# Kernel tuning notes

Measured on AMD Instinct MI355X. Metric: run time of the kernel, lower is better.

## Reference

```python
import jax, jax.numpy as jnp
import numpy as np

L, H, NH, KVH, HD, DFF = 8, 1024, 16, 2, 64, 4096
G = NH // KVH          # kv groups = 8
S, PAST = 256, 2048
T = S + PAST
QKH = NH + KVH         # heads that receive RoPE


def setup_inputs() -> dict:
    key = jax.random.key(0)
    ks = jax.random.split(key, 10)
    w = 0.02
    # causal additive mask: past fully visible, causal within new chunk
    pos = jnp.arange(T)[None, :]
    mask = jnp.where(pos <= PAST + jnp.arange(S)[:, None], 0.0, -1e9).astype(jnp.float32)
    return {
        "hidden_states": jax.random.normal(ks[0], (S, H), jnp.float32),
        "rope_cos": jax.random.uniform(ks[1], (S, 1, HD), jnp.float32, -1.0, 1.0),
        "rope_sin": jax.random.uniform(ks[2], (S, 1, HD), jnp.float32, -1.0, 1.0),
        "attention_mask": mask,
        "past_keys": jax.random.normal(ks[3], (L, KVH, HD, PAST), jnp.float32),
        "past_values": jax.random.normal(ks[4], (L, KVH, PAST, HD), jnp.float32),
        "qkv_w": jax.random.normal(ks[5], (L, (NH + 2 * KVH) * HD, H), jnp.float32) * w,
        "o_w": jax.random.normal(ks[6], (L, H, H), jnp.float32) * w,
        "gate_up_w": jax.random.normal(ks[7], (L, 2 * DFF, H), jnp.float32) * w,
        "down_w": jax.random.normal(ks[8], (L, H, DFF), jnp.float32) * w,
        "norm_w": jnp.ones((H,), jnp.float32),
    }


def _rms_sum(x):
    # faithful to module: rsqrt of SUM of squares (sqrt(H) absorbed into fused weights)
    return x * jax.lax.rsqrt(jnp.sum(x * x, axis=-1, keepdims=True))


def _rotate_half(x):
    # flip-based rotate: swaps halves, NO negation (sign folded into sin input)
    return jnp.concatenate([x[..., HD // 2:], x[..., : HD // 2]], axis=-1)


def reference(hidden_states, rope_cos, rope_sin, attention_mask,
              past_keys, past_values, qkv_w, o_w, gate_up_w, down_w, norm_w):
    def layer(h, p):
        qw, ow, guw, dw, pk, pv = p
        # --- attention ---
        x = _rms_sum(h)
        qkv = (x @ qw.T).reshape(S, NH + 2 * KVH, HD)
        qk, v = qkv[:, :QKH], qkv[:, QKH:]               # [S,QKH,HD], [S,KVH,HD]
        qk = qk * rope_cos + _rotate_half(qk) * rope_sin
        q, k = qk[:, :NH], qk[:, NH:]
        q = q.reshape(S, KVH, G, HD).transpose(1, 2, 0, 3)       # [KVH,G,S,HD]
        K = jnp.concatenate([pk, k.transpose(1, 2, 0)], axis=-1)  # [KVH,HD,T]
        V = jnp.concatenate([pv, v.transpose(1, 0, 2)], axis=-2)  # [KVH,T,HD]
        scores = jnp.einsum('kgsd,kdt->kgst', q, K) + attention_mask
        p_attn = jax.nn.softmax(scores, axis=-1)
        o = jnp.einsum('kgst,ktd->kgsd', p_attn, V)
        o = o.transpose(2, 0, 1, 3).reshape(S, H)
        h = h + o @ ow.T
        # --- fused gate-up MLP (SiLU) ---
        x = _rms_sum(h)
        gu = x @ guw.T
        gate, up = gu[:, :DFF], gu[:, DFF:]
        h = h + (jax.nn.silu(gate) * up) @ dw.T
        return h, (K, V)

    h, _kv = jax.lax.scan(layer, hidden_states,
                          (qkv_w, o_w, gate_up_w, down_w, past_keys, past_values))
    # final RMSNorm (standard, mean-based, with learned weight)
    out = h * jax.lax.rsqrt(jnp.mean(h * h, axis=-1, keepdims=True) + 1e-6) * norm_w
    return out
```

## Files before the change

### kernel.cpp

```cpp
#include <hip/hip_runtime.h>
#include <hip/hip_bf16.h>

typedef __attribute__((ext_vector_type(4))) float f32x4;
typedef __attribute__((ext_vector_type(8))) __bf16 bf16x8;
typedef unsigned short u16;
typedef __attribute__((ext_vector_type(4))) unsigned short u16x4;

__device__ __forceinline__ u16 f2bf(float f) {
  __bf16 h = (__bf16)f;
  return __builtin_bit_cast(u16, h);
}

__device__ __forceinline__ bf16x8 cvt2(f32x4 x, f32x4 y) {
  bf16x8 r;
  r[0] = (__bf16)x[0]; r[1] = (__bf16)x[1]; r[2] = (__bf16)x[2]; r[3] = (__bf16)x[3];
  r[4] = (__bf16)y[0]; r[5] = (__bf16)y[1]; r[6] = (__bf16)y[2]; r[7] = (__bf16)y[3];
  return r;
}

template<int CMODE, int NBK, int MI>
__global__ __launch_bounds__(512) void gemmW(
    const u16* __restrict__ A, const float* __restrict__ B,
    void* __restrict__ Cv, int K, int ldc)
{
  __shared__ char Bl[2][8192];
  int n0 = blockIdx.x * 32;
  int kb = blockIdx.y * (NBK * 128);
  int m0 = blockIdx.z * (MI * 128);
  int tid = threadIdx.x, lane = tid & 63, w = tid >> 6;
  int r0 = lane & 15, g = lane >> 4;
  int trow = tid >> 4, tcol = tid & 15;

  const float* bsrc = B + (long long)(n0 + trow) * K + kb + tcol * 8;
  const u16* abase = A + (long long)(m0 + w * (MI * 16) + r0) * K + kb + g * 8;
  int swr = (trow & 7) << 4;
  int wofs = trow * 256 + ((tcol * 16) ^ swr);

  {
    f32x4 u = *(const f32x4*)bsrc;
    f32x4 v = *(const f32x4*)(bsrc + 4);
    *(bf16x8*)&Bl[0][wofs] = cvt2(u, v);
  }
  bf16x8 a[2][MI][4];
#pragma unroll
  for (int mi = 0; mi < MI; mi++)
#pragma unroll
    for (int kk = 0; kk < 4; kk++)
      a[0][mi][kk] = *(const bf16x8*)(abase + (long long)mi * 16 * K + kk * 32);

  f32x4 acc[MI][2];
#pragma unroll
  for (int i = 0; i < MI; i++)
#pragma unroll
    for (int j = 0; j < 2; j++) acc[i][j] = (f32x4){0.f, 0.f, 0.f, 0.f};

  __syncthreads();

#pragma unroll
  for (int ibk = 0; ibk < NBK; ibk++) {
    const int cur = ibk & 1;
    const int nxt = cur ^ 1;
    f32x4 u, v;
    if (ibk + 1 < NBK) {
      int ko = (ibk + 1) * 128;
#pragma unroll
      for (int mi = 0; mi < MI; mi++)
#pragma unroll
        for (int kk = 0; kk < 4; kk++)
          a[nxt][mi][kk] = *(const bf16x8*)(abase + (long long)mi * 16 * K + ko + kk * 32);
      u = *(const f32x4*)(bsrc + ko);
      v = *(const f32x4*)(bsrc + ko + 4);
    }
    bf16x8 bfr[2][4];
#pragma unroll
    for (int nj = 0; nj < 2; nj++) {
      int row = nj * 16 + r0;
      int rb = row * 256, sw = (row & 7) << 4;
#pragma unroll
      for (int kk = 0; kk < 4; kk++)
        bfr[nj][kk] = *(const bf16x8*)&Bl[cur][rb + ((kk * 64 + g * 16) ^ sw)];
    }
#pragma unroll
    for (int kk = 0; kk < 4; kk++)
#pragma unroll
      for (int mi = 0; mi < MI; mi++)
#pragma unroll
        for (int nj = 0; nj < 2; nj++)
          acc[mi][nj] = __builtin_amdgcn_mfma_f32_16x16x32_bf16(a[cur][mi][kk], bfr[nj][kk], acc[mi][nj], 0, 0, 0);
    if (ibk + 1 < NBK)
      *(bf16x8*)&Bl[nxt][wofs] = cvt2(u, v);
    __syncthreads();
  }

  long long co = (long long)blockIdx.y * 256 * ldc;
  int rr = (lane >> 4) << 2;
#pragma unroll
  for (int mi = 0; mi < MI; mi++)
#pragma unroll
    for (int nj = 0; nj < 2; nj++)
#pragma unroll
      for (int q = 0; q < 4; q++) {
        int row = m0 + w * (MI * 16) + mi * 16 + rr + q;
        long long idx = co + (long long)row * ldc + n0 + nj * 16 + r0;
        float vv = acc[mi][nj][q];
        if (CMODE == 0) ((float*)Cv)[idx] = vv;
        else            ((u16*)Cv)[idx] = f2bf(vv);
      }
}

__global__ __launch_bounds__(512) void gemmGU(
    const u16* __restrict__ A, const float* __restrict__ B,
    u16* __restrict__ y)
{
  const int K = 1024, NBK = 8;
  __shared__ char Bl[2][8192];
  int n0 = blockIdx.x * 16;
  int m0 = blockIdx.y * 128;
  int tid = threadIdx.x, lane = tid & 63, w = tid >> 6;
  int r0 = lane & 15, g = lane >> 4;
  int trow = tid >> 4, tcol = tid & 15;

  const float* brow = (trow < 16)
      ? (B + (long long)(n0 + trow) * K)
      : (B + (long long)(4096 + n0 + trow - 16) * K);
  const float* bsrc = brow + tcol * 8;
  const u16* abase = A + (long long)(m0 + w * 16 + r0) * K + g * 8;
  int swr = (trow & 7) << 4;
  int wofs = trow * 256 + ((tcol * 16) ^ swr);

  {
    f32x4 u = *(const f32x4*)bsrc;
    f32x4 v = *(const f32x4*)(bsrc + 4);
    *(bf16x8*)&Bl[0][wofs] = cvt2(u, v);
  }
  bf16x8 a[2][4];
#pragma unroll
  for (int kk = 0; kk < 4; kk++)
    a[0][kk] = *(const bf16x8*)(abase + kk * 32);

  f32x4 acc[2];
  acc[0] = (f32x4){0.f, 0.f, 0.f, 0.f};
  acc[1] = (f32x4){0.f, 0.f, 0.f, 0.f};

  __syncthreads();

#pragma unroll
  for (int ibk = 0; ibk < NBK; ibk++) {
    const int cur = ibk & 1;
    const int nxt = cur ^ 1;
    f32x4 u, v;
    if (ibk + 1 < NBK) {
      int ko = (ibk + 1) * 128;
#pragma unroll
      for (int kk = 0; kk < 4; kk++)
        a[nxt][kk] = *(const bf16x8*)(abase + ko + kk * 32);
      u = *(const f32x4*)(bsrc + ko);
      v = *(const f32x4*)(bsrc + ko + 4);
    }
    bf16x8 bfr[2][4];
#pragma unroll
    for (int nj = 0; nj < 2; nj++) {
      int row = nj * 16 + r0;
      int rb = row * 256, sw = (row & 7) << 4;
#pragma unroll
      for (int kk = 0; kk < 4; kk++)
        bfr[nj][kk] = *(const bf16x8*)&Bl[cur][rb + ((kk * 64 + g * 16) ^ sw)];
    }
#pragma unroll
    for (int kk = 0; kk < 4; kk++)
#pragma unroll
      for (int nj = 0; nj < 2; nj++)
        acc[nj] = __builtin_amdgcn_mfma_f32_16x16x32_bf16(a[cur][kk], bfr[nj][kk], acc[nj], 0, 0, 0);
    if (ibk + 1 < NBK)
      *(bf16x8*)&Bl[nxt][wofs] = cvt2(u, v);
    __syncthreads();
  }

  int rr = (lane >> 4) << 2;
#pragma unroll
  for (int q = 0; q < 4; q++) {
    int row = m0 + w * 16 + rr + q;
    float gv = acc[0][q], uv = acc[1][q];
    y[(long long)row * 4096 + n0 + r0] = f2bf((gv / (1.0f + __expf(-gv))) * uv);
  }
}

__global__ __launch_bounds__(256) void rms_fuse(const float* __restrict__ src,
                                                const float* __restrict__ parts, int np,
                                                float* __restrict__ hout, u16* __restrict__ x) {
  int s = blockIdx.x, tid = threadIdx.x;
  __shared__ float red[4];
  f32x4 hv = ((const f32x4*)(src + s * 1024))[tid];
  for (int p = 0; p < np; p++) {
    f32x4 pv = ((const f32x4*)(parts + (long long)p * 262144 + s * 1024))[tid];
    hv[0] += pv[0]; hv[1] += pv[1]; hv[2] += pv[2]; hv[3] += pv[3];
  }
  float ss = hv[0]*hv[0] + hv[1]*hv[1] + hv[2]*hv[2] + hv[3]*hv[3];
#pragma unroll
  for (int off = 32; off > 0; off >>= 1) ss += __shfl_xor(ss, off, 64);
  int lane = tid & 63, w = tid >> 6;
  if (lane == 0) red[w] = ss;
  __syncthreads();
  ss = red[0] + red[1] + red[2] + red[3];
  float r = 1.0f / sqrtf(ss);
  ((f32x4*)(hout + s * 1024))[tid] = hv;
  u16x4 o;
#pragma unroll
  for (int c = 0; c < 4; c++) o[c] = f2bf(hv[c] * r);
  ((u16x4*)x)[s * 256 + tid] = o;
}

__global__ __launch_bounds__(256) void final_fuse(const float* __restrict__ src,
                                                  const float* __restrict__ parts, int np,
                                                  const float* __restrict__ nw,
                                                  float* __restrict__ out) {
  int s = blockIdx.x, tid = threadIdx.x;
  __shared__ float red[4];
  f32x4 hv = ((const f32x4*)(src + s * 1024))[tid];
  for (int p = 0; p < np; p++) {
    f32x4 pv = ((const f32x4*)(parts + (long long)p * 262144 + s * 1024))[tid];
    hv[0] += pv[0]; hv[1] += pv[1]; hv[2] += pv[2]; hv[3] += pv[3];
  }
  float ss = hv[0]*hv[0] + hv[1]*hv[1] + hv[2]*hv[2] + hv[3]*hv[3];
#pragma unroll
  for (int off = 32; off > 0; off >>= 1) ss += __shfl_xor(ss, off, 64);
  int lane = tid & 63, w = tid >> 6;
  if (lane == 0) red[w] = ss;
  __syncthreads();
  ss = red[0] + red[1] + red[2] + red[3];
  float r = 1.0f / sqrtf(ss * (1.0f / 1024.0f) + 1e-6f);
  f32x4 wv = ((const f32x4*)nw)[tid];
  f32x4 o; o[0]=hv[0]*r*wv[0]; o[1]=hv[1]*r*wv[1]; o[2]=hv[2]*r*wv[2]; o[3]=hv[3]*r*wv[3];
  ((f32x4*)(out + s * 1024))[tid] = o;
}

__global__ __launch_bounds__(256) void transpose_past(const float* __restrict__ pk,
                                                      const float* __restrict__ pv,
                                                      u16* __restrict__ Kb, u16* __restrict__ Vb) {
  __shared__ float tile[64][65];
  int t0 = blockIdx.x * 64;
  int kvh = blockIdx.y;
  int l = blockIdx.z >> 1, part = blockIdx.z & 1;
  int lk = l * 2 + kvh;
  int tid = threadIdx.x;
  if (part == 0) {
    const float* src = pk + (long long)lk * 64 * 2048;
#pragma unroll
    for (int r = 0; r < 16; r++) {
      int idx = r * 256 + tid; int d = idx >> 6, t = idx & 63;
      tile[d][t] = src[d * 2048 + t0 + t];
    }
    __syncthreads();
    u16* dst = Kb + (long long)lk * 2304 * 64;
#pragma unroll
    for (int r = 0; r < 16; r++) {
      int idx = r * 256 + tid; int t = idx >> 6, d = idx & 63;
      dst[(t0 + t) * 64 + d] = f2bf(tile[d][t]);
    }
  } else {
    const float* src = pv + (long long)lk * 2048 * 64;
#pragma unroll
    for (int r = 0; r < 16; r++) {
      int idx = r * 256 + tid; int t = idx >> 6, d = idx & 63;
      tile[t][d] = src[(t0 + t) * 64 + d];
    }
    __syncthreads();
    u16* dst = Vb + (long long)lk * 64 * 2304;
#pragma unroll
    for (int r = 0; r < 16; r++) {
      int idx = r * 256 + tid; int d = idx >> 6, t = idx & 63;
      dst[d * 2304 + t0 + t] = f2bf(tile[t][d]);
    }
  }
}

__global__ __launch_bounds__(256) void rope_qkv(const float* __restrict__ P,
                                                const float* __restrict__ cs,
                                                const float* __restrict__ sn,
                                                u16* __restrict__ qb,
                                                u16* __restrict__ Kb,
                                                u16* __restrict__ Vb) {
  int s = blockIdx.x, tid = threadIdx.x;
  long long o0 = (long long)s * 1280;
  for (int i = tid; i < 1280; i += 256) {
    int hh = i >> 6, d = i & 63;
    float v = P[o0 + i] + P[327680 + o0 + i] + P[655360 + o0 + i] + P[983040 + o0 + i];
    if (hh < 18) {
      int j = (hh << 6) | ((d + 32) & 63);
      float vr = P[o0 + j] + P[327680 + o0 + j] + P[655360 + o0 + j] + P[983040 + o0 + j];
      v = v * cs[s * 64 + d] + vr * sn[s * 64 + d];
      if (hh < 16) qb[hh * 16384 + s * 64 + d] = f2bf(v);
      else         Kb[(hh - 16) * 147456 + (2048 + s) * 64 + d] = f2bf(v);
    } else {
      Vb[(hh - 18) * 147456 + d * 2304 + 2048 + s] = f2bf(v);
    }
  }
}

struct KV { bf16x8 kf[2][2]; bf16x8 vf[4]; };

__global__ __launch_bounds__(512) void flash_attn(
    const u16* __restrict__ qb, const u16* __restrict__ Kb2,
    const u16* __restrict__ Vb2, u16* __restrict__ oacc)
{
  __shared__ u16 Plds[8][16][36];
  __shared__ float Osh[8][16][68];
  __shared__ float msh[8][16];
  __shared__ float lsh[8][16];

  int hh = blockIdx.y, kvh = hh >> 3;
  int s0 = blockIdx.x * 16;
  int tid = threadIdx.x, lane = tid & 63, w = tid >> 6;
  int g = lane >> 4, r0 = lane & 15;

  const u16* Q  = qb  + hh * (256 * 64);
  const u16* Kh = Kb2 + kvh * (2304 * 64);
  const u16* Vh = Vb2 + kvh * (64 * 2304);

  bf16x8 qf[2];
#pragma unroll
  for (int kk = 0; kk < 2; kk++)
    qf[kk] = *(const bf16x8*)(Q + (s0 + r0) * 64 + kk * 32 + g * 8);

  f32x4 O[4];
#pragma unroll
  for (int dj = 0; dj < 4; dj++) O[dj] = (f32x4){0.f, 0.f, 0.f, 0.f};
  float m = -1e30f, l = 0.f;

  int t0s = w * 288;

  auto loadkv = [&](KV& d, int t0) {
#pragma unroll
    for (int tj = 0; tj < 2; tj++)
#pragma unroll
      for (int kk = 0; kk < 2; kk++)
        d.kf[tj][kk] = *(const bf16x8*)(Kh + (t0 + tj * 16 + r0) * 64 + kk * 32 + g * 8);
#pragma unroll
    for (int dj = 0; dj < 4; dj++)
      d.vf[dj] = *(const bf16x8*)(Vh + (dj * 16 + r0) * 2304 + t0 + g * 8);
  };

  auto step = [&](KV& kv, int t0) {
    f32x4 sc[2];
#pragma unroll
    for (int tj = 0; tj < 2; tj++) {
      f32x4 z = (f32x4){0.f, 0.f, 0.f, 0.f};
      z = __builtin_amdgcn_mfma_f32_16x16x32_bf16(kv.kf[tj][0], qf[0], z, 0, 0, 0);
      z = __builtin_amdgcn_mfma_f32_16x16x32_bf16(kv.kf[tj][1], qf[1], z, 0, 0, 0);
      sc[tj] = z;
    }
    if (t0 + 31 > 2048 + s0) {
#pragma unroll
      for (int tj = 0; tj < 2; tj++)
#pragma unroll
        for (int q = 0; q < 4; q++) {
          int tg = t0 + tj * 16 + g * 4 + q;
          int sg = s0 + r0;
          if (tg > 2048 + sg) sc[tj][q] = -1e30f;
        }
    }
    float rm = -1e30f;
#pragma unroll
    for (int tj = 0; tj < 2; tj++)
#pragma unroll
      for (int q = 0; q < 4; q++) rm = fmaxf(rm, sc[tj][q]);
    rm = fmaxf(rm, __shfl_xor(rm, 16, 64));
    rm = fmaxf(rm, __shfl_xor(rm, 32, 64));
    float mn = fmaxf(m, rm);
    float sca = __expf(m - mn);
    float rs = 0.f;
#pragma unroll
    for (int tj = 0; tj < 2; tj++)
#pragma unroll
      for (int q = 0; q < 4; q++) {
        sc[tj][q] = __expf(sc[tj][q] - mn);
        rs += sc[tj][q];
      }
    rs += __shfl_xor(rs, 16, 64);
    rs += __shfl_xor(rs, 32, 64);
    l = l * sca + rs;
    m = mn;
#pragma unroll
    for (int dj = 0; dj < 4; dj++) {
      O[dj][0] *= sca; O[dj][1] *= sca; O[dj][2] *= sca; O[dj][3] *= sca;
    }
#pragma unroll
    for (int tj = 0; tj < 2; tj++) {
      u16x4 pw;
#pragma unroll
      for (int q = 0; q < 4; q++) pw[q] = f2bf(sc[tj][q]);
      *(u16x4*)&Plds[w][r0][tj * 16 + g * 4] = pw;
    }
    u16x4 plo = *(const u16x4*)&Plds[w][r0][g * 8];
    u16x4 phi = *(const u16x4*)&Plds[w][r0][g * 8 + 4];
    union { bf16x8 v; u16x4 h[2]; } pu;
    pu.h[0] = plo; pu.h[1] = phi;
#pragma unroll
    for (int dj = 0; dj < 4; dj++)
      O[dj] = __builtin_amdgcn_mfma_f32_16x16x32_bf16(kv.vf[dj], pu.v, O[dj], 0, 0, 0);
  };

  KV ba, bb;
  loadkv(ba, t0s);
#pragma unroll 1
  for (int p = 0; p < 4; p++) {
    int t0 = t0s + p * 64;
    loadkv(bb, t0 + 32);
    step(ba, t0);
    loadkv(ba, t0 + 64);
    step(bb, t0 + 32);
  }
  step(ba, t0s + 256);

#pragma unroll
  for (int dj = 0; dj < 4; dj++)
    *(f32x4*)&Osh[w][r0][dj * 16 + g * 4] = O[dj];
  if (g == 0) { msh[w][r0] = m; lsh[w][r0] = l; }
  __syncthreads();

  if (tid < 256) {
    int row = tid >> 4, c0 = (tid & 15) * 4;
    float M = -1e30f;
#pragma unroll
    for (int w8 = 0; w8 < 8; w8++) M = fmaxf(M, msh[w8][row]);
    float L = 0.f;
    float a0 = 0.f, a1 = 0.f, a2 = 0.f, a3 = 0.f;
#pragma unroll
    for (int w8 = 0; w8 < 8; w8++) {
      float e = __expf(msh[w8][row] - M);
      L += lsh[w8][row] * e;
      f32x4 ov = *(const f32x4*)&Osh[w8][row][c0];
      a0 += e * ov[0]; a1 += e * ov[1]; a2 += e * ov[2]; a3 += e * ov[3];
    }
    float inv = 1.0f / L;
    u16x4 o4;
    o4[0] = f2bf(a0 * inv); o4[1] = f2bf(a1 * inv);
    o4[2] = f2bf(a2 * inv); o4[3] = f2bf(a3 * inv);
    *(u16x4*)(oacc + (long long)(s0 + row) * 1024 + hh * 64 + c0) = o4;
  }
}

extern "C" void kernel_launch(void* const* d_in, const int* in_sizes, int n_in,
                              void* d_out, int out_size, void* d_ws, size_t ws_size,
                              hipStream_t stream) {
  (void)in_sizes; (void)n_in; (void)out_size; (void)ws_size;
  const float* hs   = (const float*)d_in[0];
  const float* rc   = (const float*)d_in[1];
  const float* rs   = (const float*)d_in[2];
  const float* pk   = (const float*)d_in[4];
  const float* pv   = (const float*)d_in[5];
  const float* qkvw = (const float*)d_in[6];
  const float* ow   = (const float*)d_in[7];
  const float* guw  = (const float*)d_in[8];
  const float* dw   = (const float*)d_in[9];
  const float* nw   = (const float*)d_in[10];
  float* out = (float*)d_out;

  char* base = (char*)d_ws;
  float* h   = (float*)(base + 0);
  u16*  x    = (u16*)(base + 1048576);
  float* Pq  = (float*)(base + 1572864);
  float* Po  = (float*)(base + 6815744);
  float* Pd  = (float*)(base + 11010048);
  u16*  y    = (u16*)(base + 15204352);
  u16*  oacc = (u16*)(base + 17301504);
  u16*  qb   = (u16*)(base + 17825792);
  u16*  Kb   = (u16*)(base + 18350080);
  u16*  Vb   = (u16*)(base + 23068672);

  transpose_past<<<dim3(32, 2, 16), 256, 0, stream>>>(pk, pv, Kb, Vb);

  for (int l = 0; l < 8; ++l) {
    u16* Kbl = Kb + (long long)l * 2 * 2304 * 64;
    u16* Vbl = Vb + (long long)l * 2 * 64 * 2304;

    if (l == 0)
      rms_fuse<<<256, 256, 0, stream>>>(hs, nullptr, 0, h, x);
    else
      rms_fuse<<<256, 256, 0, stream>>>(h, Pd, 4, h, x);

    gemmW<0, 2, 1><<<dim3(40, 4, 2), 512, 0, stream>>>(
        x, qkvw + (long long)l * 1310720, Pq, 1024, 1280);
    rope_qkv<<<256, 256, 0, stream>>>(Pq, rc, rs, qb, Kbl, Vbl);
    flash_attn<<<dim3(16, 16), 512, 0, stream>>>(qb, Kbl, Vbl, oacc);
    gemmW<0, 2, 1><<<dim3(32, 4, 2), 512, 0, stream>>>(
        oacc, ow + (long long)l * 1048576, Po, 1024, 1024);
    rms_fuse<<<256, 256, 0, stream>>>(h, Po, 4, h, x);
    gemmGU<<<dim3(256, 2), 512, 0, stream>>>(
        x, guw + (long long)l * 8388608, y);
    gemmW<0, 8, 1><<<dim3(32, 4, 2), 512, 0, stream>>>(
        y, dw + (long long)l * 4194304, Pd, 4096, 1024);
  }
  final_fuse<<<256, 256, 0, stream>>>(h, Pd, 4, nw, out);
}
```

Measured before the change: 629.9 us.

## Retile weight-streaming GEMMs to narrow N tiles with full-M blocks and split-K

Result: slower. 804.3 us (+27.7%).

```diff
diff --git a/kernel.cpp b/kernel.cpp
--- a/kernel.cpp
+++ b/kernel.cpp
@@ -108,35 +108,35 @@
       }
 }
 
-__global__ __launch_bounds__(512) void gemmGU(
+template<int NBK>
+__global__ __launch_bounds__(512) void gemmW16(
     const u16* __restrict__ A, const float* __restrict__ B,
-    u16* __restrict__ y)
+    float* __restrict__ Cv, int K, int ldc)
 {
-  const int K = 1024, NBK = 8;
-  __shared__ char Bl[2][8192];
+  __shared__ char Bl[2][4096];
   int n0 = blockIdx.x * 16;
-  int m0 = blockIdx.y * 128;
+  int kb = blockIdx.y * (NBK * 128);
   int tid = threadIdx.x, lane = tid & 63, w = tid >> 6;
   int r0 = lane & 15, g = lane >> 4;
-  int trow = tid >> 4, tcol = tid & 15;
-
-  const float* brow = (trow < 16)
-      ? (B + (long long)(n0 + trow) * K)
-      : (B + (long long)(4096 + n0 + trow - 16) * K);
-  const float* bsrc = brow + tcol * 8;
-  const u16* abase = A + (long long)(m0 + w * 16 + r0) * K + g * 8;
+  int trow = (tid >> 4) & 15, tcol = tid & 15;
+  bool stager = tid < 256;
+
+  const float* bsrc = B + (long long)(n0 + trow) * K + kb + tcol * 8;
+  const u16* abase = A + (long long)(w * 32 + r0) * K + kb + g * 8;
   int swr = (trow & 7) << 4;
   int wofs = trow * 256 + ((tcol * 16) ^ swr);
 
-  {
+  if (stager) {
     f32x4 u = *(const f32x4*)bsrc;
     f32x4 v = *(const f32x4*)(bsrc + 4);
     *(bf16x8*)&Bl[0][wofs] = cvt2(u, v);
   }
-  bf16x8 a[2][4];
-#pragma unroll
-  for (int kk = 0; kk < 4; kk++)
-    a[0][kk] = *(const bf16x8*)(abase + kk * 32);
+  bf16x8 a[2][2][4];
+#pragma unroll
+  for (int mi = 0; mi < 2; mi++)
+#pragma unroll
+    for (int kk = 0; kk < 4; kk++)
+      a[0][mi][kk] = *(const bf16x8*)(abase + (long long)mi * 16 * K + kk * 32);
 
   f32x4 acc[2];
   acc[0] = (f32x4){0.f, 0.f, 0.f, 0.f};
@@ -152,37 +152,126 @@
     if (ibk + 1 < NBK) {
       int ko = (ibk + 1) * 128;
 #pragma unroll
+      for (int mi = 0; mi < 2; mi++)
+#pragma unroll
+        for (int kk = 0; kk < 4; kk++)
+          a[nxt][mi][kk] = *(const bf16x8*)(abase + (long long)mi * 16 * K + ko + kk * 32);
+      if (stager) {
+        u = *(const f32x4*)(bsrc + ko);
+        v = *(const f32x4*)(bsrc + ko + 4);
+      }
+    }
+    bf16x8 bfr[4];
+    {
+      int rb = r0 * 256, sw = (r0 & 7) << 4;
+#pragma unroll
       for (int kk = 0; kk < 4; kk++)
-        a[nxt][kk] = *(const bf16x8*)(abase + ko + kk * 32);
-      u = *(const f32x4*)(bsrc + ko);
-      v = *(const f32x4*)(bsrc + ko + 4);
-    }
-    bf16x8 bfr[2][4];
-#pragma unroll
-    for (int nj = 0; nj < 2; nj++) {
-      int row = nj * 16 + r0;
-      int rb = row * 256, sw = (row & 7) << 4;
-#pragma unroll
-      for (int kk = 0; kk < 4; kk++)
-        bfr[nj][kk] = *(const bf16x8*)&Bl[cur][rb + ((kk * 64 + g * 16) ^ sw)];
+        bfr[kk] = *(const bf16x8*)&Bl[cur][rb + ((kk * 64 + g * 16) ^ sw)];
     }
 #pragma unroll
     for (int kk = 0; kk < 4; kk++)
 #pragma unroll
-      for (int nj = 0; nj < 2; nj++)
-        acc[nj] = __builtin_amdgcn_mfma_f32_16x16x32_bf16(a[cur][kk], bfr[nj][kk], acc[nj], 0, 0, 0);
-    if (ibk + 1 < NBK)
+      for (int mi = 0; mi < 2; mi++)
+        acc[mi] = __builtin_amdgcn_mfma_f32_16x16x32_bf16(a[cur][mi][kk], bfr[kk], acc[mi], 0, 0, 0);
+    if (ibk + 1 < NBK && stager)
       *(bf16x8*)&Bl[nxt][wofs] = cvt2(u, v);
     __syncthreads();
   }
 
+  long long co = (long long)blockIdx.y * 256 * ldc;
   int rr = (lane >> 4) << 2;
 #pragma unroll
-  for (int q = 0; q < 4; q++) {
-    int row = m0 + w * 16 + rr + q;
-    float gv = acc[0][q], uv = acc[1][q];
-    y[(long long)row * 4096 + n0 + r0] = f2bf((gv / (1.0f + __expf(-gv))) * uv);
-  }
+  for (int mi = 0; mi < 2; mi++)
+#pragma unroll
+    for (int q = 0; q < 4; q++) {
+      int row = w * 32 + mi * 16 + rr + q;
+      Cv[co + (long long)row * ldc + n0 + r0] = acc[mi][q];
+    }
+}
+
+__global__ __launch_bounds__(512) void gemmGU8(
+    const u16* __restrict__ A, const float* __restrict__ B,
+    u16* __restrict__ y)
+{
+  const int K = 1024, NBK = 8;
+  __shared__ char Bl[2][4096];
+  int n0 = blockIdx.x * 8;
+  int tid = threadIdx.x, lane = tid & 63, w = tid >> 6;
+  int r0 = lane & 15, g = lane >> 4;
+  int trow = (tid >> 4) & 15, tcol = tid & 15;
+  bool stager = tid < 256;
+
+  const float* brow = (trow < 8)
+      ? (B + (long long)(n0 + trow) * K)
+      : (B + (long long)(4096 + n0 + trow - 8) * K);
+  const float* bsrc = brow + tcol * 8;
+  const u16* abase = A + (long long)(w * 32 + r0) * K + g * 8;
+  int swr = (trow & 7) << 4;
+  int wofs = trow * 256 + ((tcol * 16) ^ swr);
+
+  if (stager) {
+    f32x4 u = *(const f32x4*)bsrc;
+    f32x4 v = *(const f32x4*)(bsrc + 4);
+    *(bf16x8*)&Bl[0][wofs] = cvt2(u, v);
+  }
+  bf16x8 a[2][2][4];
+#pragma unroll
+  for (int mi = 0; mi < 2; mi++)
+#pragma unroll
+    for (int kk = 0; kk < 4; kk++)
+      a[0][mi][kk] = *(const bf16x8*)(abase + (long long)mi * 16 * K + kk * 32);
+
+  f32x4 acc[2];
+  acc[0] = (f32x4){0.f, 0.f, 0.f, 0.f};
+  acc[1] = (f32x4){0.f, 0.f, 0.f, 0.f};
+
+  __syncthreads();
+
+#pragma unroll
+  for (int ibk = 0; ibk < NBK; ibk++) {
+    const int cur = ibk & 1;
+    const int nxt = cur ^ 1;
+    f32x4 u, v;
+    if (ibk + 1 < NBK) {
+      int ko = (ibk + 1) * 128;
+#pragma unroll
+      for (int mi = 0; mi < 2; mi++)
+#pragma unroll
+        for (int kk = 0; kk < 4; kk++)
+          a[nxt][mi][kk] = *(const bf16x8*)(abase + ko + (long long)mi * 16 * K + kk * 32);
+      if (stager) {
+        u = *(const f32x4*)(bsrc + ko);
+        v = *(const f32x4*)(bsrc + ko + 4);
+      }
+    }
+    bf16x8 bfr[4];
+    {
+      int rb = r0 * 256, sw = (r0 & 7) << 4;
+#pragma unroll
+      for (int kk = 0; kk < 4; kk++)
+        bfr[kk] = *(const bf16x8*)&Bl[cur][rb + ((kk * 64 + g * 16) ^ sw)];
+    }
+#pragma unroll
+    for (int kk = 0; kk < 4; kk++)
+#pragma unroll
+      for (int mi = 0; mi < 2; mi++)
+        acc[mi] = __builtin_amdgcn_mfma_f32_16x16x32_bf16(a[cur][mi][kk], bfr[kk], acc[mi], 0, 0, 0);
+    if (ibk + 1 < NBK && stager)
+      *(bf16x8*)&Bl[nxt][wofs] = cvt2(u, v);
+    __syncthreads();
+  }
+
+  int rr = (lane >> 4) << 2;
+#pragma unroll
+  for (int mi = 0; mi < 2; mi++)
+#pragma unroll
+    for (int q = 0; q < 4; q++) {
+      int row = w * 32 + mi * 16 + rr + q;
+      float v = acc[mi][q];
+      float other = __shfl_xor(v, 8, 64);
+      if (r0 < 8)
+        y[(long long)row * 4096 + n0 + r0] = f2bf((v / (1.0f + __expf(-v))) * other);
+    }
 }
 
 __global__ __launch_bounds__(256) void rms_fuse(const float* __restrict__ src,
@@ -462,11 +551,11 @@
   float* Pq  = (float*)(base + 1572864);
   float* Po  = (float*)(base + 6815744);
   float* Pd  = (float*)(base + 11010048);
-  u16*  y    = (u16*)(base + 15204352);
-  u16*  oacc = (u16*)(base + 17301504);
-  u16*  qb   = (u16*)(base + 17825792);
-  u16*  Kb   = (u16*)(base + 18350080);
-  u16*  Vb   = (u16*)(base + 23068672);
+  u16*  y    = (u16*)(base + 19398656);
+  u16*  oacc = (u16*)(base + 21495808);
+  u16*  qb   = (u16*)(base + 22020096);
+  u16*  Kb   = (u16*)(base + 22544384);
+  u16*  Vb   = (u16*)(base + 27262976);
 
   transpose_past<<<dim3(32, 2, 16), 256, 0, stream>>>(pk, pv, Kb, Vb);
 
@@ -477,19 +566,19 @@
     if (l == 0)
       rms_fuse<<<256, 256, 0, stream>>>(hs, nullptr, 0, h, x);
     else
-      rms_fuse<<<256, 256, 0, stream>>>(h, Pd, 4, h, x);
-
-    gemmW<0, 2, 1><<<dim3(40, 4, 2), 512, 0, stream>>>(
+      rms_fuse<<<256, 256, 0, stream>>>(h, Pd, 8, h, x);
+
+    gemmW16<2><<<dim3(80, 4), 512, 0, stream>>>(
         x, qkvw + (long long)l * 1310720, Pq, 1024, 1280);
     rope_qkv<<<256, 256, 0, stream>>>(Pq, rc, rs, qb, Kbl, Vbl);
     flash_attn<<<dim3(16, 16), 512, 0, stream>>>(qb, Kbl, Vbl, oacc);
     gemmW<0, 2, 1><<<dim3(32, 4, 2), 512, 0, stream>>>(
         oacc, ow + (long long)l * 1048576, Po, 1024, 1024);
     rms_fuse<<<256, 256, 0, stream>>>(h, Po, 4, h, x);
-    gemmGU<<<dim3(256, 2), 512, 0, stream>>>(
+    gemmGU8<<<dim3(512), 512, 0, stream>>>(
         x, guw + (long long)l * 8388608, y);
-    gemmW<0, 8, 1><<<dim3(32, 4, 2), 512, 0, stream>>>(
+    gemmW16<4><<<dim3(64, 8), 512, 0, stream>>>(
         y, dw + (long long)l * 4194304, Pd, 4096, 1024);
   }
-  final_fuse<<<256, 256, 0, stream>>>(h, Pd, 4, nw, out);
-}
+  final_fuse<<<256, 256, 0, stream>>>(h, Pd, 8, nw, out);
+}
```

## Restructure gate-up GEMM to stage activations in LDS and stream weights via registers

Applied to the files above, without the earlier changes.

Result: slower. 755.8 us (+20.0%).

```diff
diff --git a/kernel.cpp b/kernel.cpp
--- a/kernel.cpp
+++ b/kernel.cpp
@@ -108,81 +108,100 @@
       }
 }
 
-__global__ __launch_bounds__(512) void gemmGU(
+__global__ __launch_bounds__(512) void gemmGUbs(
     const u16* __restrict__ A, const float* __restrict__ B,
     u16* __restrict__ y)
 {
-  const int K = 1024, NBK = 8;
-  __shared__ char Bl[2][8192];
+  __shared__ u16 Al[2][32768];
   int n0 = blockIdx.x * 16;
-  int m0 = blockIdx.y * 128;
   int tid = threadIdx.x, lane = tid & 63, w = tid >> 6;
   int r0 = lane & 15, g = lane >> 4;
-  int trow = tid >> 4, tcol = tid & 15;
-
-  const float* brow = (trow < 16)
-      ? (B + (long long)(n0 + trow) * K)
-      : (B + (long long)(4096 + n0 + trow - 16) * K);
-  const float* bsrc = brow + tcol * 8;
-  const u16* abase = A + (long long)(m0 + w * 16 + r0) * K + g * 8;
-  int swr = (trow & 7) << 4;
-  int wofs = trow * 256 + ((tcol * 16) ^ swr);
-
-  {
-    f32x4 u = *(const f32x4*)bsrc;
-    f32x4 v = *(const f32x4*)(bsrc + 4);
-    *(bf16x8*)&Bl[0][wofs] = cvt2(u, v);
-  }
-  bf16x8 a[2][4];
-#pragma unroll
-  for (int kk = 0; kk < 4; kk++)
-    a[0][kk] = *(const bf16x8*)(abase + kk * 32);
-
-  f32x4 acc[2];
-  acc[0] = (f32x4){0.f, 0.f, 0.f, 0.f};
-  acc[1] = (f32x4){0.f, 0.f, 0.f, 0.f};
-
+
+  const float* bg = B + (long long)(n0 + r0) * 1024 + g * 8;
+  const float* bu = B + (long long)(4096 + n0 + r0) * 1024 + g * 8;
+
+  int sofs[8];
+  const u16* asrc[8];
+#pragma unroll
+  for (int j = 0; j < 8; j++) {
+    int id = j * 512 + tid;
+    int srow = id >> 4;
+    int c16 = id & 15;
+    sofs[j] = srow * 128 + ((((c16 * 16) ^ ((srow & 7) << 4))) >> 1);
+    asrc[j] = A + (long long)srow * 1024 + c16 * 8;
+  }
+
+  f32x4 Bg[2][4][2], Bu[2][4][2];
+  f32x4 acc[2][2];
+#pragma unroll
+  for (int i = 0; i < 2; i++)
+#pragma unroll
+    for (int j = 0; j < 2; j++) acc[i][j] = (f32x4){0.f, 0.f, 0.f, 0.f};
+
+#pragma unroll
+  for (int j = 0; j < 8; j++)
+    *(bf16x8*)&Al[0][sofs[j]] = *(const bf16x8*)(asrc[j]);
+#pragma unroll
+  for (int kk = 0; kk < 4; kk++) {
+    Bg[0][kk][0] = *(const f32x4*)(bg + kk * 32);
+    Bg[0][kk][1] = *(const f32x4*)(bg + kk * 32 + 4);
+    Bu[0][kk][0] = *(const f32x4*)(bu + kk * 32);
+    Bu[0][kk][1] = *(const f32x4*)(bu + kk * 32 + 4);
+  }
   __syncthreads();
 
 #pragma unroll
-  for (int ibk = 0; ibk < NBK; ibk++) {
-    const int cur = ibk & 1;
+  for (int slab = 0; slab < 8; slab++) {
+    const int cur = slab & 1;
     const int nxt = cur ^ 1;
-    f32x4 u, v;
-    if (ibk + 1 < NBK) {
-      int ko = (ibk + 1) * 128;
-#pragma unroll
-      for (int kk = 0; kk < 4; kk++)
-        a[nxt][kk] = *(const bf16x8*)(abase + ko + kk * 32);
-      u = *(const f32x4*)(bsrc + ko);
-      v = *(const f32x4*)(bsrc + ko + 4);
-    }
-    bf16x8 bfr[2][4];
-#pragma unroll
-    for (int nj = 0; nj < 2; nj++) {
-      int row = nj * 16 + r0;
-      int rb = row * 256, sw = (row & 7) << 4;
-#pragma unroll
-      for (int kk = 0; kk < 4; kk++)
-        bfr[nj][kk] = *(const bf16x8*)&Bl[cur][rb + ((kk * 64 + g * 16) ^ sw)];
-    }
-#pragma unroll
-    for (int kk = 0; kk < 4; kk++)
-#pragma unroll
-      for (int nj = 0; nj < 2; nj++)
-        acc[nj] = __builtin_amdgcn_mfma_f32_16x16x32_bf16(a[cur][kk], bfr[nj][kk], acc[nj], 0, 0, 0);
-    if (ibk + 1 < NBK)
-      *(bf16x8*)&Bl[nxt][wofs] = cvt2(u, v);
+    bf16x8 ast[8];
+    if (slab < 7) {
+      int kb2 = (slab + 1) * 128;
+#pragma unroll
+      for (int j = 0; j < 8; j++)
+        ast[j] = *(const bf16x8*)(asrc[j] + kb2);
+#pragma unroll
+      for (int kk = 0; kk < 4; kk++) {
+        Bg[nxt][kk][0] = *(const f32x4*)(bg + kb2 + kk * 32);
+        Bg[nxt][kk][1] = *(const f32x4*)(bg + kb2 + kk * 32 + 4);
+        Bu[nxt][kk][0] = *(const f32x4*)(bu + kb2 + kk * 32);
+        Bu[nxt][kk][1] = *(const f32x4*)(bu + kb2 + kk * 32 + 4);
+      }
+    }
+#pragma unroll
+    for (int kk = 0; kk < 4; kk++) {
+      bf16x8 af[2];
+#pragma unroll
+      for (int mi = 0; mi < 2; mi++) {
+        int row = w * 32 + mi * 16 + r0;
+        int c16 = kk * 4 + g;
+        af[mi] = *(const bf16x8*)&Al[cur][row * 128 + ((((c16 * 16) ^ ((row & 7) << 4))) >> 1)];
+      }
+      bf16x8 gq = cvt2(Bg[cur][kk][0], Bg[cur][kk][1]);
+      bf16x8 uq = cvt2(Bu[cur][kk][0], Bu[cur][kk][1]);
+#pragma unroll
+      for (int mi = 0; mi < 2; mi++) {
+        acc[mi][0] = __builtin_amdgcn_mfma_f32_16x16x32_bf16(af[mi], gq, acc[mi][0], 0, 0, 0);
+        acc[mi][1] = __builtin_amdgcn_mfma_f32_16x16x32_bf16(af[mi], uq, acc[mi][1], 0, 0, 0);
+      }
+    }
+    if (slab < 7) {
+#pragma unroll
+      for (int j = 0; j < 8; j++)
+        *(bf16x8*)&Al[nxt][sofs[j]] = ast[j];
+    }
     __syncthreads();
   }
 
   int rr = (lane >> 4) << 2;
 #pragma unroll
-  for (int q = 0; q < 4; q++) {
-    int row = m0 + w * 16 + rr + q;
-    float gv = acc[0][q], uv = acc[1][q];
-    y[(long long)row * 4096 + n0 + r0] = f2bf((gv / (1.0f + __expf(-gv))) * uv);
-  }
+  for (int mi = 0; mi < 2; mi++)
+#pragma unroll
+    for (int q = 0; q < 4; q++) {
+      int row = w * 32 + mi * 16 + rr + q;
+      float gv = acc[mi][0][q], uv = acc[mi][1][q];
+      y[(long long)row * 4096 + n0 + r0] = f2bf((gv / (1.0f + __expf(-gv))) * uv);
+    }
 }
 
 __global__ __launch_bounds__(256) void rms_fuse(const float* __restrict__ src,
@@ -486,7 +505,7 @@
     gemmW<0, 2, 1><<<dim3(32, 4, 2), 512, 0, stream>>>(
         oacc, ow + (long long)l * 1048576, Po, 1024, 1024);
     rms_fuse<<<256, 256, 0, stream>>>(h, Po, 4, h, x);
-    gemmGU<<<dim3(256, 2), 512, 0, stream>>>(
+    gemmGUbs<<<dim3(256), 512, 0, stream>>>(
         x, guw + (long long)l * 8388608, y);
     gemmW<0, 8, 1><<<dim3(32, 4, 2), 512, 0, stream>>>(
         y, dw + (long long)l * 4194304, Pd, 4096, 1024);
```

## Pre-convert all weights to bf16 once and use bf16-input GEMM kernels

Applied to the files above, without the earlier changes.

After: 716.3 us. +13.7%, slower.

```diff
diff --git a/kernel.cpp b/kernel.cpp
--- a/kernel.cpp
+++ b/kernel.cpp
@@ -16,6 +16,16 @@
   r[0] = (__bf16)x[0]; r[1] = (__bf16)x[1]; r[2] = (__bf16)x[2]; r[3] = (__bf16)x[3];
   r[4] = (__bf16)y[0]; r[5] = (__bf16)y[1]; r[6] = (__bf16)y[2]; r[7] = (__bf16)y[3];
   return r;
+}
+
+__global__ __launch_bounds__(256) void cvt_w(const float* __restrict__ s,
+                                             u16* __restrict__ d, int n8) {
+  int stride = gridDim.x * 256;
+  for (int i = blockIdx.x * 256 + threadIdx.x; i < n8; i += stride) {
+    f32x4 a = ((const f32x4*)s)[i * 2];
+    f32x4 b = ((const f32x4*)s)[i * 2 + 1];
+    *(bf16x8*)(d + (long long)i * 8) = cvt2(a, b);
+  }
 }
 
 template<int CMODE, int NBK, int MI>
@@ -106,6 +116,175 @@
         if (CMODE == 0) ((float*)Cv)[idx] = vv;
         else            ((u16*)Cv)[idx] = f2bf(vv);
       }
+}
+
+template<int CMODE, int NSL>
+__global__ __launch_bounds__(512) void gemmWB(
+    const u16* __restrict__ A, const u16* __restrict__ Bw,
+    void* __restrict__ Cv, int K, int ldc)
+{
+  __shared__ char Bl[2][16384];
+  int n0 = blockIdx.x * 32;
+  int kb = blockIdx.y * (NSL * 256);
+  int m0 = blockIdx.z * 128;
+  int tid = threadIdx.x, lane = tid & 63, w = tid >> 6;
+  int r0 = lane & 15, g = lane >> 4;
+  int trow = tid >> 4, tc = tid & 15;
+
+  const u16* bsrc = Bw + (long long)(n0 + trow) * K + kb + tc * 16;
+  const u16* abase = A + (long long)(m0 + w * 16 + r0) * K + kb + g * 8;
+  int swr = (trow & 7) << 4;
+  int sofsA = trow * 512 + ((tc * 32) ^ swr);
+  int sofsB = trow * 512 + ((tc * 32 + 16) ^ swr);
+
+  *(bf16x8*)&Bl[0][sofsA] = *(const bf16x8*)bsrc;
+  *(bf16x8*)&Bl[0][sofsB] = *(const bf16x8*)(bsrc + 8);
+
+  bf16x8 aH0[4];
+#pragma unroll
+  for (int kk = 0; kk < 4; kk++)
+    aH0[kk] = *(const bf16x8*)(abase + kk * 32);
+
+  f32x4 acc[2];
+  acc[0] = (f32x4){0.f, 0.f, 0.f, 0.f};
+  acc[1] = (f32x4){0.f, 0.f, 0.f, 0.f};
+
+  __syncthreads();
+
+#pragma unroll
+  for (int s = 0; s < NSL; s++) {
+    const int cur = s & 1;
+    const int nxt = cur ^ 1;
+    bf16x8 aH1[4], aN0[4], bp0, bp1;
+#pragma unroll
+    for (int kk = 0; kk < 4; kk++)
+      aH1[kk] = *(const bf16x8*)(abase + s * 256 + 128 + kk * 32);
+    if (s + 1 < NSL) {
+      int ko = (s + 1) * 256;
+      bp0 = *(const bf16x8*)(bsrc + ko);
+      bp1 = *(const bf16x8*)(bsrc + ko + 8);
+#pragma unroll
+      for (int kk = 0; kk < 4; kk++)
+        aN0[kk] = *(const bf16x8*)(abase + ko + kk * 32);
+    }
+#pragma unroll
+    for (int h = 0; h < 2; h++) {
+#pragma unroll
+      for (int kk = 0; kk < 4; kk++) {
+        bf16x8 af = h == 0 ? aH0[kk] : aH1[kk];
+#pragma unroll
+        for (int nj = 0; nj < 2; nj++) {
+          int row = nj * 16 + r0;
+          int j = h * 16 + kk * 4 + g;
+          bf16x8 bf = *(const bf16x8*)&Bl[cur][row * 512 + ((j * 16) ^ ((row & 7) << 4))];
+          acc[nj] = __builtin_amdgcn_mfma_f32_16x16x32_bf16(af, bf, acc[nj], 0, 0, 0);
+        }
+      }
+    }
+    if (s + 1 < NSL) {
+      *(bf16x8*)&Bl[nxt][sofsA] = bp0;
+      *(bf16x8*)&Bl[nxt][sofsB] = bp1;
+#pragma unroll
+      for (int kk = 0; kk < 4; kk++) aH0[kk] = aN0[kk];
+    }
+    __syncthreads();
+  }
+
+  long long co = (long long)blockIdx.y * 256 * ldc;
+  int rr = (lane >> 4) << 2;
+#pragma unroll
+  for (int nj = 0; nj < 2; nj++)
+#pragma unroll
+    for (int q = 0; q < 4; q++) {
+      int row = m0 + w * 16 + rr + q;
+      long long idx = co + (long long)row * ldc + n0 + nj * 16 + r0;
+      float vv = acc[nj][q];
+      if (CMODE == 0) ((float*)Cv)[idx] = vv;
+      else            ((u16*)Cv)[idx] = f2bf(vv);
+    }
+}
+
+__global__ __launch_bounds__(512) void gemmGUB(
+    const u16* __restrict__ A, const u16* __restrict__ Bw,
+    u16* __restrict__ y)
+{
+  const int K = 1024, NSL = 4;
+  __shared__ char Bl[2][16384];
+  int n0 = blockIdx.x * 16;
+  int m0 = blockIdx.y * 128;
+  int tid = threadIdx.x, lane = tid & 63, w = tid >> 6;
+  int r0 = lane & 15, g = lane >> 4;
+  int trow = tid >> 4, tc = tid & 15;
+
+  const u16* brow = (trow < 16)
+      ? (Bw + (long long)(n0 + trow) * K)
+      : (Bw + (long long)(4096 + n0 + trow - 16) * K);
+  const u16* bsrc = brow + tc * 16;
+  const u16* abase = A + (long long)(m0 + w * 16 + r0) * K + g * 8;
+  int swr = (trow & 7) << 4;
+  int sofsA = trow * 512 + ((tc * 32) ^ swr);
+  int sofsB = trow * 512 + ((tc * 32 + 16) ^ swr);
+
+  *(bf16x8*)&Bl[0][sofsA] = *(const bf16x8*)bsrc;
+  *(bf16x8*)&Bl[0][sofsB] = *(const bf16x8*)(bsrc + 8);
+
+  bf16x8 aH0[4];
+#pragma unroll
+  for (int kk = 0; kk < 4; kk++)
+    aH0[kk] = *(const bf16x8*)(abase + kk * 32);
+
+  f32x4 acc[2];
+  acc[0] = (f32x4){0.f, 0.f, 0.f, 0.f};
+  acc[1] = (f32x4){0.f, 0.f, 0.f, 0.f};
+
+  __syncthreads();
+
+#pragma unroll
+  for (int s = 0; s < NSL; s++) {
+    const int cur = s & 1;
+    const int nxt = cur ^ 1;
+    bf16x8 aH1[4], aN0[4], bp0, bp1;
+#pragma unroll
+    for (int kk = 0; kk < 4; kk++)
+      aH1[kk] = *(const bf16x8*)(abase + s * 256 + 128 + kk * 32);
+    if (s + 1 < NSL) {
+      int ko = (s + 1) * 256;
+      bp0 = *(const bf16x8*)(bsrc + ko);
+      bp1 = *(const bf16x8*)(bsrc + ko + 8);
+#pragma unroll
+      for (int kk = 0; kk < 4; kk++)
+        aN0[kk] = *(const bf16x8*)(abase + ko + kk * 32);
+    }
+#pragma unroll
+    for (int h = 0; h < 2; h++) {
+#pragma unroll
+      for (int kk = 0; kk < 4; kk++) {
+        bf16x8 af = h == 0 ? aH0[kk] : aH1[kk];
+#pragma unroll
+        for (int nj = 0; nj < 2; nj++) {
+          int row = nj * 16 + r0;
+          int j = h * 16 + kk * 4 + g;
+          bf16x8 bf = *(const bf16x8*)&Bl[cur][row * 512 + ((j * 16) ^ ((row & 7) << 4))];
+          acc[nj] = __builtin_amdgcn_mfma_f32_16x16x32_bf16(af, bf, acc[nj], 0, 0, 0);
+        }
+      }
+    }
+    if (s + 1 < NSL) {
+      *(bf16x8*)&Bl[nxt][sofsA] = bp0;
+      *(bf16x8*)&Bl[nxt][sofsB] = bp1;
+#pragma unroll
+      for (int kk = 0; kk < 4; kk++) aH0[kk] = aN0[kk];
+    }
+    __syncthreads();
+  }
+
+  int rr = (lane >> 4) << 2;
+#pragma unroll
+  for (int q = 0; q < 4; q++) {
+    int row = m0 + w * 16 + rr + q;
+    float gv = acc[0][q], uv = acc[1][q];
+    y[(long long)row * 4096 + n0 + r0] = f2bf((gv / (1.0f + __expf(-gv))) * uv);
+  }
 }
 
 __global__ __launch_bounds__(512) void gemmGU(
@@ -443,7 +622,7 @@
 extern "C" void kernel_launch(void* const* d_in, const int* in_sizes, int n_in,
                               void* d_out, int out_size, void* d_ws, size_t ws_size,
                               hipStream_t stream) {
-  (void)in_sizes; (void)n_in; (void)out_size; (void)ws_size;
+  (void)in_sizes; (void)n_in; (void)out_size;
   const float* hs   = (const float*)d_in[0];
   const float* rc   = (const float*)d_in[1];
   const float* rs   = (const float*)d_in[2];
@@ -467,7 +646,18 @@
   u16*  qb   = (u16*)(base + 17825792);
   u16*  Kb   = (u16*)(base + 18350080);
   u16*  Vb   = (u16*)(base + 23068672);
-
+  u16*  qkvwB = (u16*)(base + 33554432);
+  u16*  owB   = (u16*)(base + 54525952);
+  u16*  guwB  = (u16*)(base + 71303168);
+  u16*  dwB   = (u16*)(base + 205520896);
+  const bool BF16W = ws_size >= 272629760ULL;
+
+  if (BF16W) {
+    cvt_w<<<2048, 256, 0, stream>>>(qkvw, qkvwB, 1310720);
+    cvt_w<<<2048, 256, 0, stream>>>(ow, owB, 1048576);
+    cvt_w<<<8192, 256, 0, stream>>>(guw, guwB, 8388608);
+    cvt_w<<<4096, 256, 0, stream>>>(dw, dwB, 4194304);
+  }
   transpose_past<<<dim3(32, 2, 16), 256, 0, stream>>>(pk, pv, Kb, Vb);
 
   for (int l = 0; l < 8; ++l) {
@@ -479,17 +669,34 @@
     else
       rms_fuse<<<256, 256, 0, stream>>>(h, Pd, 4, h, x);
 
-    gemmW<0, 2, 1><<<dim3(40, 4, 2), 512, 0, stream>>>(
-        x, qkvw + (long long)l * 1310720, Pq, 1024, 1280);
+    if (BF16W) {
+      gemmWB<0, 1><<<dim3(40, 4, 2), 512, 0, stream>>>(
+          x, qkvwB + (long long)l * 1310720, Pq, 1024, 1280);
+    } else {
+      gemmW<0, 2, 1><<<dim3(40, 4, 2), 512, 0, stream>>>(
+          x, qkvw + (long long)l * 1310720, Pq, 1024, 1280);
+    }
     rope_qkv<<<256, 256, 0, stream>>>(Pq, rc, rs, qb, Kbl, Vbl);
     flash_attn<<<dim3(16, 16), 512, 0, stream>>>(qb, Kbl, Vbl, oacc);
-    gemmW<0, 2, 1><<<dim3(32, 4, 2), 512, 0, stream>>>(
-        oacc, ow + (long long)l * 1048576, Po, 1024, 1024);
+    if (BF16W) {
+      gemmWB<0, 1><<<dim3(32, 4, 2), 512, 0, stream>>>(
+          oacc, owB + (long long)l * 1048576, Po, 1024, 1024);
+    } else {
+      gemmW<0, 2, 1><<<dim3(32, 4, 2), 512, 0, stream>>>(
+          oacc, ow + (long long)l * 1048576, Po, 1024, 1024);
+    }
     rms_fuse<<<256, 256, 0, stream>>>(h, Po, 4, h, x);
-    gemmGU<<<dim3(256, 2), 512, 0, stream>>>(
-        x, guw + (long long)l * 8388608, y);
-    gemmW<0, 8, 1><<<dim3(32, 4, 2), 512, 0, stream>>>(
-        y, dw + (long long)l * 4194304, Pd, 4096, 1024);
+    if (BF16W) {
+      gemmGUB<<<dim3(256, 2), 512, 0, stream>>>(
+          x, guwB + (long long)l * 8388608, y);
+      gemmWB<0, 4><<<dim3(32, 4, 2), 512, 0, stream>>>(
+          y, dwB + (long long)l * 4194304, Pd, 4096, 1024);
+    } else {
+      gemmGU<<<dim3(256, 2), 512, 0, stream>>>(
+          x, guw + (long long)l * 8388608, y);
+      gemmW<0, 8, 1><<<dim3(32, 4, 2), 512, 0, stream>>>(
+          y, dw + (long long)l * 4194304, Pd, 4096, 1024);
+    }
   }
   final_fuse<<<256, 256, 0, stream>>>(h, Pd, 4, nw, out);
 }
```
